# Kernel tuning notes

Hardware: AMD Instinct MI355X
Metric: run time of the kernel (lower is better)

## Reference

```python
import jax, jax.numpy as jnp
import numpy as np

B, T, E, L, V = 16, 1024, 768, 2, 50257
LN_EPS = 1e-5


def setup_inputs() -> dict:
    key = jax.random.key(0)
    ks = jax.random.split(key, 5)
    idx = jax.random.randint(ks[0], (B, T), 0, V)
    wte = jax.random.normal(ks[1], (V, E), dtype=jnp.float32) * 0.02
    Wih = jax.random.normal(ks[2], (L, 3 * E, E), dtype=jnp.float32) * 0.02
    Whh = jax.random.normal(ks[3], (L, 3 * E, E), dtype=jnp.float32) * 0.02
    bih = jnp.zeros((L, 3 * E), dtype=jnp.float32)
    bhh = jnp.zeros((L, 3 * E), dtype=jnp.float32)
    g = jnp.ones((E,), dtype=jnp.float32)
    return {"idx": idx, "wte": wte, "Wih": Wih, "bih": bih,
            "Whh": Whh, "bhh": bhh, "g": g}


def _gru_forward(idx, wte, Wih, bih, Whh, bhh, g):
    x = wte[idx]                       # [B,T,E] token embeddings (dropout=0 -> identity)

    def step(h, xt):                   # h: [L,B,E], xt: [B,E]
        inp = xt
        new_h = []
        for l in range(L):             # small fixed layer loop
            gi = inp @ Wih[l].T + bih[l]       # [B,3E]
            gh = h[l] @ Whh[l].T + bhh[l]      # [B,3E]
            i_r, i_z, i_n = jnp.split(gi, 3, axis=-1)
            h_r, h_z, h_n = jnp.split(gh, 3, axis=-1)
            r = jax.nn.sigmoid(i_r + h_r)
            z = jax.nn.sigmoid(i_z + h_z)
            n = jnp.tanh(i_n + r * h_n)
            hl = (1.0 - z) * n + z * h[l]
            new_h.append(hl)
            inp = hl
        return jnp.stack(new_h), inp   # carry, top-layer output at this t

    h0 = jnp.zeros((L, B, E), dtype=x.dtype)
    _, outs = jax.lax.scan(step, h0, jnp.swapaxes(x, 0, 1))  # outs: [T,B,E]

    # targets=None path: LayerNorm (no bias) + lm_head on the LAST position only
    last = outs[-1]                    # [B,E]
    mu = jnp.mean(last, axis=-1, keepdims=True)
    var = jnp.mean(jnp.square(last - mu), axis=-1, keepdims=True)
    ln = (last - mu) * jax.lax.rsqrt(var + LN_EPS) * g
    logits = ln @ wte.T                # tied lm_head, [B,V]
    return logits[:, None, :]          # [B,1,V]


def reference(idx, wte, Wih, bih, Whh, bhh, g):
    return _gru_forward(idx, wte, Wih, bih, Whh, bhh, g)
```

## Files before the change

kernel.cpp:

```cpp
#include <hip/hip_runtime.h>
#include <hip/hip_fp16.h>
#include <math.h>

#define Bz 16
#define Tz 1024
#define Ez 768
#define E3 2304
#define Vz 50257
#define NBK 256
#define LN_EPS 1e-5f
#define VEC (Bz*Ez)
#define VECW 6144
#define EP 772
#define BS 8
#define CW 12

__device__ __forceinline__ float dot4acc(float acc, float4 w, float4 h){
  acc = fmaf(w.x,h.x,acc); acc = fmaf(w.y,h.y,acc);
  acc = fmaf(w.z,h.z,acc); acc = fmaf(w.w,h.w,acc);
  return acc;
}
__device__ __forceinline__ float sigm(float x){ return 1.0f/(1.0f+expf(-x)); }

__device__ __forceinline__ unsigned pack2(float a, float b){
  __half2 h = __floats2half2_rn(a, b);
  union{__half2 h2; unsigned u;} cv; cv.h2 = h; return cv.u;
}
__device__ __forceinline__ float2 unpack2(unsigned u){
  union{unsigned u; __half2 h2;} cv; cv.u = u;
  return __half22float2(cv.h2);
}


__device__ __forceinline__ void stage8(const unsigned* __restrict__ src,
                                       float (*dst)[EP], int tid){
#pragma unroll
  for (int k=0;k<2;k++){
    const int u0 = tid + k*1536;
    const int u1 = u0 + 512;
    const int u2 = u0 + 1024;
    const unsigned a0 = __hip_atomic_load(src+u0, __ATOMIC_RELAXED, __HIP_MEMORY_SCOPE_AGENT);
    const unsigned a1 = __hip_atomic_load(src+u1, __ATOMIC_RELAXED, __HIP_MEMORY_SCOPE_AGENT);
    const unsigned a2 = __hip_atomic_load(src+u2, __ATOMIC_RELAXED, __HIP_MEMORY_SCOPE_AGENT);
    {const int b=u0/384, c=(u0-b*384)<<1; const float2 f=unpack2(a0); dst[b][c]=f.x; dst[b][c+1]=f.y;}
    {const int b=u1/384, c=(u1-b*384)<<1; const float2 f=unpack2(a1); dst[b][c]=f.x; dst[b][c+1]=f.y;}
    {const int b=u2/384, c=(u2-b*384)<<1; const float2 f=unpack2(a2); dst[b][c]=f.x; dst[b][c+1]=f.y;}
  }
}

__device__ __forceinline__ void zero8(float (*dst)[EP], int tid){
#pragma unroll
  for (int k=0;k<6;k++){
    const int u = tid + (k<<9);
    const int b = u/384, c = (u-b*384)<<1;
    dst[b][c] = 0.f; dst[b][c+1] = 0.f;
  }
}

__device__ __forceinline__ void mm6(const float (*V)[EP],
                                    const float* const (&wRow)[6],
                                    float (*gOut)[9],
                                    int wv, int kq, int bb){
  float acc[6][2];
#pragma unroll
  for (int r=0;r<6;r++){ acc[r][0]=0.f; acc[r][1]=0.f; }
#pragma unroll 4
  for (int j=0;j<12;j++){
    const int kk = (j<<6) + (kq<<2);
    float4 w4[6];
#pragma unroll
    for (int r=0;r<6;r++) w4[r] = *(const float4*)(wRow[r] + kk);
#pragma unroll
    for (int bi=0;bi<2;bi++){
      const float4 hv = *(const float4*)&V[bb*2+bi][kk];
#pragma unroll
      for (int r=0;r<6;r++) acc[r][bi] = dot4acc(acc[r][bi], w4[r], hv);
    }
  }
#pragma unroll
  for (int r=0;r<6;r++)
#pragma unroll
    for (int bi=0;bi<2;bi++){
      float a = acc[r][bi];
      a += __shfl_xor(a,1); a += __shfl_xor(a,2);
      a += __shfl_xor(a,4); a += __shfl_xor(a,8);
      acc[r][bi]=a;
    }
  if (kq==0){
#pragma unroll
    for (int r=0;r<6;r++)
#pragma unroll
      for (int bi=0;bi<2;bi++) gOut[wv*6+r][bb*2+bi] = acc[r][bi];
  }
}

__global__ __launch_bounds__(512) void gru_scan(
    const int* __restrict__ idx, const float* __restrict__ wte,
    const float* __restrict__ Wih, const float* __restrict__ bih,
    const float* __restrict__ Whh, const float* __restrict__ bhh,
    unsigned* __restrict__ h0g, unsigned* __restrict__ h1g,
    float* __restrict__ h1f,
    unsigned* __restrict__ flags, unsigned* __restrict__ go)
{
  __shared__ float bufX[BS][EP];
  __shared__ float bufH[BS][EP];
  __shared__ float gatesI[36][9];
  __shared__ float gatesG[36][9];
  __shared__ float biasS[72];
  __shared__ float hprev[BS][CW];

  const int tid = threadIdx.x, bx = blockIdx.x;
  const int L = bx>>7, sub = bx&127;
  const int bg = sub>>6, cg = sub&63;
  const int c0 = cg*CW, b0 = bg*BS;
  const int wv = tid>>6, lane = tid&63, kq = lane&15, bb = lane>>4;

  const float* WihL = Wih + (size_t)L*E3*Ez;
  const float* WhhL = Whh + (size_t)L*E3*Ez;

  const float* wiRow[6];
  const float* whRow[6];
#pragma unroll
  for (int r=0;r<6;r++){
    const int m = (wv<6 ? wv : 0)*6 + r, g = m/12, cc = m - g*12;
    wiRow[r] = WihL + (size_t)(g*Ez + c0 + cc)*Ez;
    whRow[r] = WhhL + (size_t)(g*Ez + c0 + cc)*Ez;
  }
  if (tid<72){
    const int mat = tid/36, mm = tid%36, g = mm/12, cc = mm-g*12;
    biasS[tid] = (mat ? bhh : bih)[L*E3 + g*Ez + c0 + cc];
  }
  if (tid<96) hprev[tid&7][tid>>3] = 0.f;

  if (L==0){
#pragma unroll
    for (int k=0;k<3;k++){
      const int i4 = tid + (k<<9);
      const int b = i4/192, c4 = i4 - b*192;
      const int row = idx[(b0+b)*Tz];
      *(float4*)&bufX[b][c4<<2] = *(const float4*)(wte + (size_t)row*Ez + (c4<<2));
    }
    __syncthreads();
    if (wv<6) mm6(bufX, wiRow, gatesI, wv, kq, bb);
  }
  __syncthreads();

  for (int s=0; s<=Tz+1; ++s){
    if (s>0){
      const unsigned tgt = (unsigned)s;
      if (bx==0){
        if (tid<64){
          const unsigned* f = flags + (tid<<2);
          for(;;){
            const unsigned a0 = __hip_atomic_load(f+0, __ATOMIC_RELAXED, __HIP_MEMORY_SCOPE_AGENT);
            const unsigned a1 = __hip_atomic_load(f+1, __ATOMIC_RELAXED, __HIP_MEMORY_SCOPE_AGENT);
            const unsigned a2 = __hip_atomic_load(f+2, __ATOMIC_RELAXED, __HIP_MEMORY_SCOPE_AGENT);
            const unsigned a3 = __hip_atomic_load(f+3, __ATOMIC_RELAXED, __HIP_MEMORY_SCOPE_AGENT);
            const int ok = (a0>=tgt) & (a1>=tgt) & (a2>=tgt) & (a3>=tgt);
            if (__all(ok)) break;
            __builtin_amdgcn_s_sleep(1);
          }
          __hip_atomic_store(go + (tid<<5), tgt,
                             __ATOMIC_RELAXED, __HIP_MEMORY_SCOPE_AGENT);
        }
      } else {
        if (tid==0){
          const unsigned* gp = go + ((bx&63)<<5);
          while (__hip_atomic_load(gp, __ATOMIC_RELAXED, __HIP_MEMORY_SCOPE_AGENT) < tgt)
            __builtin_amdgcn_s_sleep(2);
        }
      }
      __syncthreads();
    }

    const bool activeC = (L==0) ? (s<Tz) : (s>=2);
    if (activeC){
      if (L==0){
        if (s==0) zero8(bufH, tid);
        else      stage8(h0g + (size_t)((s-1)%3)*VECW + bg*3072, bufH, tid);
      } else {
        if (s==2) zero8(bufH, tid);
        else      stage8(h1g + (size_t)((s-1)&1)*VECW + bg*3072, bufH, tid);
      }
      __syncthreads();
      if (wv<6) mm6(bufH, whRow, gatesG, wv, kq, bb);
      __syncthreads();

      if (tid<48){
        const int b = tid&7, j = tid>>3;
        float hv2[2];
#pragma unroll
        for (int e=0;e<2;e++){
          const int cc = 2*j+e;
          const float gir = gatesI[cc    ][b] + biasS[cc];
          const float giz = gatesI[12+cc][b] + biasS[12+cc];
          const float gin = gatesI[24+cc][b] + biasS[24+cc];
          const float ghr = gatesG[cc    ][b] + biasS[36+cc];
          const float ghz = gatesG[12+cc][b] + biasS[48+cc];
          const float ghn = gatesG[24+cc][b] + biasS[60+cc];
          const float r = sigm(gir+ghr);
          const float z = sigm(giz+ghz);
          const float n = tanhf(fmaf(r, ghn, gin));
          const float hp = hprev[b][cc];
          hv2[e] = fmaf(z, hp - n, n);
          hprev[b][cc] = hv2[e];
        }
        unsigned* hOutW = (L==0) ? (h0g + (size_t)(s%3)*VECW)
                                 : (h1g + (size_t)(s&1)*VECW);
        const unsigned pk = pack2(hv2[0], hv2[1]);
        __hip_atomic_store(hOutW + (b0+b)*384 + cg*6 + j, pk,
                           __ATOMIC_RELAXED, __HIP_MEMORY_SCOPE_AGENT);
        if (L==1 && s==Tz+1){
          h1f[(b0+b)*Ez + c0 + 2*j    ] = hv2[0];
          h1f[(b0+b)*Ez + c0 + 2*j + 1] = hv2[1];
        }
      }
    }

    __syncthreads();
    if (tid==0)
      __hip_atomic_store(flags + bx, (unsigned)(s+1),
                         __ATOMIC_RELAXED, __HIP_MEMORY_SCOPE_AGENT);

    const bool activeE = (L==0) ? (s < Tz-1) : (s>=1 && s<=Tz);
    if (activeE){
      if (L==0){
#pragma unroll
        for (int k=0;k<3;k++){
          const int i4 = tid + (k<<9);
          const int b = i4/192, c4 = i4 - b*192;
          const int row = idx[(b0+b)*Tz + (s+1)];
          *(float4*)&bufX[b][c4<<2] = *(const float4*)(wte + (size_t)row*Ez + (c4<<2));
        }
      } else {
        stage8(h0g + (size_t)((s-1)%3)*VECW + bg*3072, bufX, tid);
      }
      __syncthreads();
      if (wv<6) mm6(bufX, wiRow, gatesI, wv, kq, bb);
    }
  }
}

__global__ __launch_bounds__(256) void finalize_ln(
    const float* __restrict__ h1, const float* __restrict__ g,
    float* __restrict__ ln)
{
  const int tid=threadIdx.x, wv=tid>>6, lane=tid&63;
  for (int b=wv; b<Bz; b+=4){
    float sum=0.f;
    for (int c=lane;c<Ez;c+=64) sum += h1[b*Ez+c];
#pragma unroll
    for (int off=32; off; off>>=1) sum += __shfl_xor(sum, off);
    const float mu = sum/(float)Ez;
    float s2=0.f;
    for (int c=lane;c<Ez;c+=64){ const float d=h1[b*Ez+c]-mu; s2=fmaf(d,d,s2); }
#pragma unroll
    for (int off=32; off; off>>=1) s2 += __shfl_xor(s2, off);
    const float inv = rsqrtf(s2/(float)Ez + LN_EPS);
    for (int c=lane;c<Ez;c+=64) ln[b*Ez+c] = (h1[b*Ez+c]-mu)*inv*g[c];
  }
}

__global__ __launch_bounds__(256) void lm_head(
    const float* __restrict__ ln, const float* __restrict__ wte,
    float* __restrict__ out)
{
  __shared__ float sLn[Bz][EP];
  const int tid=threadIdx.x;
  for (int i4=tid; i4<Bz*Ez/4; i4+=256){
    const int b = i4/(Ez/4), c = (i4 - b*(Ez/4))<<2;
    *(float4*)(&sLn[b][c]) = *(const float4*)(ln + b*Ez + c);
  }
  __syncthreads();
  const int wv=tid>>6, lane=tid&63, rr=lane>>4, cl=lane&15;
  const int vbase = blockIdx.x*64 + wv*16 + rr;
  float acc[4][16];
#pragma unroll
  for (int k=0;k<4;k++)
#pragma unroll
    for (int b=0;b<16;b++) acc[k][b]=0.f;

  for (int j=0;j<12;j++){
    const int c = (cl<<2) + (j<<6);
    float4 w4[4];
#pragma unroll
    for (int k=0;k<4;k++){
      const int v = vbase + 4*k;
      if (v < Vz) w4[k] = *(const float4*)(wte + (size_t)v*Ez + c);
      else { w4[k].x=w4[k].y=w4[k].z=w4[k].w=0.f; }
    }
#pragma unroll
    for (int b=0;b<16;b++){
      const float4 hv = *(const float4*)(&sLn[b][c]);
#pragma unroll
      for (int k=0;k<4;k++) acc[k][b] = dot4acc(acc[k][b], w4[k], hv);
    }
  }
#pragma unroll
  for (int off=1; off<16; off<<=1)
#pragma unroll
    for (int k=0;k<4;k++)
#pragma unroll
      for (int b=0;b<16;b++) acc[k][b] += __shfl_xor(acc[k][b], off);

  if (cl==0){
#pragma unroll
    for (int k=0;k<4;k++){
      const int v = vbase + 4*k;
      if (v < Vz){
#pragma unroll
        for (int b=0;b<16;b++) out[(size_t)b*Vz + v] = acc[k][b];
      }
    }
  }
}

extern "C" void kernel_launch(void* const* d_in, const int* in_sizes, int n_in,
                              void* d_out, int out_size, void* d_ws, size_t ws_size,
                              hipStream_t stream) {
  const int*   idx = (const int*)  d_in[0];
  const float* wte = (const float*)d_in[1];
  const float* Wih = (const float*)d_in[2];
  const float* bih = (const float*)d_in[3];
  const float* Whh = (const float*)d_in[4];
  const float* bhh = (const float*)d_in[5];
  const float* g   = (const float*)d_in[6];
  float* out = (float*)d_out;

  unsigned* flags = (unsigned*)d_ws;
  unsigned* go    = (unsigned*)d_ws + 512;
  unsigned* h0g   = (unsigned*)d_ws + 4096;
  unsigned* h1g   = h0g + 3*VECW;
  float*    h1f   = (float*)(h1g + 2*VECW);
  float*    ln    = h1f + VEC;

  (void)hipMemsetAsync(d_ws, 0, 16384, stream);

  void* args[] = {(void*)&idx,(void*)&wte,(void*)&Wih,(void*)&bih,
                  (void*)&Whh,(void*)&bhh,(void*)&h0g,(void*)&h1g,
                  (void*)&h1f,(void*)&flags,(void*)&go};
  (void)hipLaunchCooperativeKernel((void*)gru_scan, dim3(NBK), dim3(512), args, 0, stream);

  finalize_ln<<<1, 256, 0, stream>>>(h1f, g, ln);
  lm_head<<<786, 256, 0, stream>>>(ln, wte, out);
}
```

Baseline: 12.99 ms.

## Run input and hidden GEMVs concurrently on separate waves with double-buffered gates

All 8 waves now work each step: waves 0-3 compute the hidden-to-hidden gates (9 rows each) while waves 4-7 compute the input-to-hidden gates for the next step, using a double-buffered gatesI array. Before, only 6 waves ran, and they did the two matvecs one after the other. For layer 1 the staging of x and h is merged into one pass, and the layer-0 embedding prefetch moves one step further ahead. This shortens the serial critical path per step, at the cost of more complex step indexing and more registers for 9-row accumulators.

```diff
diff --git a/kernel.cpp b/kernel.cpp
--- a/kernel.cpp
+++ b/kernel.cpp
@@ -48,6 +48,27 @@
   }
 }
 
+__device__ __forceinline__ void stage8x2(const unsigned* __restrict__ srcX,
+                                         float (*dstX)[EP],
+                                         const unsigned* __restrict__ srcH,
+                                         float (*dstH)[EP], int tid){
+#pragma unroll
+  for (int k=0;k<3;k++){
+    const int u0 = tid + (k<<10);
+    const int u1 = u0 + 512;
+    const unsigned x0 = __hip_atomic_load(srcX+u0, __ATOMIC_RELAXED, __HIP_MEMORY_SCOPE_AGENT);
+    const unsigned x1 = __hip_atomic_load(srcX+u1, __ATOMIC_RELAXED, __HIP_MEMORY_SCOPE_AGENT);
+    const unsigned h0 = __hip_atomic_load(srcH+u0, __ATOMIC_RELAXED, __HIP_MEMORY_SCOPE_AGENT);
+    const unsigned h1 = __hip_atomic_load(srcH+u1, __ATOMIC_RELAXED, __HIP_MEMORY_SCOPE_AGENT);
+    const int b0=u0/384, c0_=(u0-b0*384)<<1;
+    const int b1=u1/384, c1_=(u1-b1*384)<<1;
+    {const float2 f=unpack2(x0); dstX[b0][c0_]=f.x; dstX[b0][c0_+1]=f.y;}
+    {const float2 f=unpack2(x1); dstX[b1][c1_]=f.x; dstX[b1][c1_+1]=f.y;}
+    {const float2 f=unpack2(h0); dstH[b0][c0_]=f.x; dstH[b0][c0_+1]=f.y;}
+    {const float2 f=unpack2(h1); dstH[b1][c1_]=f.x; dstH[b1][c1_+1]=f.y;}
+  }
+}
+
 __device__ __forceinline__ void zero8(float (*dst)[EP], int tid){
 #pragma unroll
   for (int k=0;k<6;k++){
@@ -57,28 +78,28 @@
   }
 }
 
-__device__ __forceinline__ void mm6(const float (*V)[EP],
-                                    const float* const (&wRow)[6],
+__device__ __forceinline__ void mm9(const float (*V)[EP],
+                                    const float* const (&wRow)[9],
                                     float (*gOut)[9],
-                                    int wv, int kq, int bb){
-  float acc[6][2];
-#pragma unroll
-  for (int r=0;r<6;r++){ acc[r][0]=0.f; acc[r][1]=0.f; }
+                                    int wv4, int kq, int bb){
+  float acc[9][2];
+#pragma unroll
+  for (int r=0;r<9;r++){ acc[r][0]=0.f; acc[r][1]=0.f; }
 #pragma unroll 4
   for (int j=0;j<12;j++){
     const int kk = (j<<6) + (kq<<2);
-    float4 w4[6];
-#pragma unroll
-    for (int r=0;r<6;r++) w4[r] = *(const float4*)(wRow[r] + kk);
+    float4 w4[9];
+#pragma unroll
+    for (int r=0;r<9;r++) w4[r] = *(const float4*)(wRow[r] + kk);
 #pragma unroll
     for (int bi=0;bi<2;bi++){
       const float4 hv = *(const float4*)&V[bb*2+bi][kk];
 #pragma unroll
-      for (int r=0;r<6;r++) acc[r][bi] = dot4acc(acc[r][bi], w4[r], hv);
-    }
-  }
-#pragma unroll
-  for (int r=0;r<6;r++)
+      for (int r=0;r<9;r++) acc[r][bi] = dot4acc(acc[r][bi], w4[r], hv);
+    }
+  }
+#pragma unroll
+  for (int r=0;r<9;r++)
 #pragma unroll
     for (int bi=0;bi<2;bi++){
       float a = acc[r][bi];
@@ -88,9 +109,9 @@
     }
   if (kq==0){
 #pragma unroll
-    for (int r=0;r<6;r++)
-#pragma unroll
-      for (int bi=0;bi<2;bi++) gOut[wv*6+r][bb*2+bi] = acc[r][bi];
+    for (int r=0;r<9;r++)
+#pragma unroll
+      for (int bi=0;bi<2;bi++) gOut[wv4*9+r][bb*2+bi] = acc[r][bi];
   }
 }
 
@@ -104,8 +125,8 @@
 {
   __shared__ float bufX[BS][EP];
   __shared__ float bufH[BS][EP];
-  __shared__ float gatesI[36][9];
   __shared__ float gatesG[36][9];
+  __shared__ float gatesI[2][36][9];
   __shared__ float biasS[72];
   __shared__ float hprev[BS][CW];
 
@@ -114,17 +135,19 @@
   const int bg = sub>>6, cg = sub&63;
   const int c0 = cg*CW, b0 = bg*BS;
   const int wv = tid>>6, lane = tid&63, kq = lane&15, bb = lane>>4;
+  const int wv4 = wv & 3;
 
   const float* WihL = Wih + (size_t)L*E3*Ez;
   const float* WhhL = Whh + (size_t)L*E3*Ez;
 
-  const float* wiRow[6];
-  const float* whRow[6];
-#pragma unroll
-  for (int r=0;r<6;r++){
-    const int m = (wv<6 ? wv : 0)*6 + r, g = m/12, cc = m - g*12;
-    wiRow[r] = WihL + (size_t)(g*Ez + c0 + cc)*Ez;
-    whRow[r] = WhhL + (size_t)(g*Ez + c0 + cc)*Ez;
+  const float* wRow[9];
+  {
+    const float* Wb = (wv < 4) ? WhhL : WihL;
+#pragma unroll
+    for (int r=0;r<9;r++){
+      const int m = wv4*9 + r, g = m/12, cc = m - g*12;
+      wRow[r] = Wb + (size_t)(g*Ez + c0 + cc)*Ez;
+    }
   }
   if (tid<72){
     const int mat = tid/36, mm = tid%36, g = mm/12, cc = mm-g*12;
@@ -141,7 +164,15 @@
       *(float4*)&bufX[b][c4<<2] = *(const float4*)(wte + (size_t)row*Ez + (c4<<2));
     }
     __syncthreads();
-    if (wv<6) mm6(bufX, wiRow, gatesI, wv, kq, bb);
+    if (wv>=4) mm9(bufX, wRow, gatesI[1], wv4, kq, bb);
+    __syncthreads();
+#pragma unroll
+    for (int k=0;k<3;k++){
+      const int i4 = tid + (k<<9);
+      const int b = i4/192, c4 = i4 - b*192;
+      const int row = idx[(b0+b)*Tz + 1];
+      *(float4*)&bufX[b][c4<<2] = *(const float4*)(wte + (size_t)row*Ez + (c4<<2));
+    }
   }
   __syncthreads();
 
@@ -173,44 +204,55 @@
       __syncthreads();
     }
 
-    const bool activeC = (L==0) ? (s<Tz) : (s>=2);
-    if (activeC){
+    const bool gG = (L==0) ? (s<=Tz-1) : (s>=2);
+    const bool gI = (L==0) ? (s<=Tz-2) : (s>=1 && s<=Tz);
+
+    if (L==0){
+      if (s==0)            zero8(bufH, tid);
+      else if (s<=Tz-1)    stage8(h0g + (size_t)((s-1)%3)*VECW + bg*3072, bufH, tid);
+    } else {
+      const unsigned* x_src = h0g + (size_t)((s-1)%3)*VECW + bg*3072;
+      const unsigned* h_src = h1g + (size_t)((s-1)&1)*VECW + bg*3072;
+      if (s>=3 && s<=Tz)      stage8x2(x_src, bufX, h_src, bufH, tid);
+      else if (s==2)        { stage8(x_src, bufX, tid); zero8(bufH, tid); }
+      else if (s==1)          stage8(x_src, bufX, tid);
+      else if (s==Tz+1)       stage8(h_src, bufH, tid);
+    }
+    __syncthreads();
+
+    if (wv<4){ if (gG) mm9(bufH, wRow, gatesG,        wv4, kq, bb); }
+    else     { if (gI) mm9(bufX, wRow, gatesI[s&1],   wv4, kq, bb); }
+    __syncthreads();
+
+    if (gG && tid<48){
+      const int b = tid&7, j = tid>>3;
+      float hv2[2];
+#pragma unroll
+      for (int e=0;e<2;e++){
+        const int cc = 2*j+e;
+        const float gir = gatesI[(s-1)&1][cc    ][b] + biasS[cc];
+        const float giz = gatesI[(s-1)&1][12+cc][b] + biasS[12+cc];
+        const float gin = gatesI[(s-1)&1][24+cc][b] + biasS[24+cc];
+        const float ghr = gatesG[cc    ][b] + biasS[36+cc];
+        const float ghz = gatesG[12+cc][b] + biasS[48+cc];
+        const float ghn = gatesG[24+cc][b] + biasS[60+cc];
+        const float r = sigm(gir+ghr);
+        const float z = sigm(giz+ghz);
+        const float n = tanhf(fmaf(r, ghn, gin));
+        const float hp = hprev[b][cc];
+        hv2[e] = fmaf(z, hp - n, n);
+        hprev[b][cc] = hv2[e];
+      }
+      const unsigned pk = pack2(hv2[0], hv2[1]);
       if (L==0){
-        if (s==0) zero8(bufH, tid);
-        else      stage8(h0g + (size_t)((s-1)%3)*VECW + bg*3072, bufH, tid);
-      } else {
-        if (s==2) zero8(bufH, tid);
-        else      stage8(h1g + (size_t)((s-1)&1)*VECW + bg*3072, bufH, tid);
-      }
-      __syncthreads();
-      if (wv<6) mm6(bufH, whRow, gatesG, wv, kq, bb);
-      __syncthreads();
-
-      if (tid<48){
-        const int b = tid&7, j = tid>>3;
-        float hv2[2];
-#pragma unroll
-        for (int e=0;e<2;e++){
-          const int cc = 2*j+e;
-          const float gir = gatesI[cc    ][b] + biasS[cc];
-          const float giz = gatesI[12+cc][b] + biasS[12+cc];
-          const float gin = gatesI[24+cc][b] + biasS[24+cc];
-          const float ghr = gatesG[cc    ][b] + biasS[36+cc];
-          const float ghz = gatesG[12+cc][b] + biasS[48+cc];
-          const float ghn = gatesG[24+cc][b] + biasS[60+cc];
-          const float r = sigm(gir+ghr);
-          const float z = sigm(giz+ghz);
-          const float n = tanhf(fmaf(r, ghn, gin));
-          const float hp = hprev[b][cc];
-          hv2[e] = fmaf(z, hp - n, n);
-          hprev[b][cc] = hv2[e];
-        }
-        unsigned* hOutW = (L==0) ? (h0g + (size_t)(s%3)*VECW)
-                                 : (h1g + (size_t)(s&1)*VECW);
-        const unsigned pk = pack2(hv2[0], hv2[1]);
+        unsigned* hOutW = h0g + (size_t)(s%3)*VECW;
         __hip_atomic_store(hOutW + (b0+b)*384 + cg*6 + j, pk,
                            __ATOMIC_RELAXED, __HIP_MEMORY_SCOPE_AGENT);
-        if (L==1 && s==Tz+1){
+      } else {
+        unsigned* hOutW = h1g + (size_t)((s-2)&1)*VECW;
+        __hip_atomic_store(hOutW + (b0+b)*384 + cg*6 + j, pk,
+                           __ATOMIC_RELAXED, __HIP_MEMORY_SCOPE_AGENT);
+        if (s==Tz+1){
           h1f[(b0+b)*Ez + c0 + 2*j    ] = hv2[0];
           h1f[(b0+b)*Ez + c0 + 2*j + 1] = hv2[1];
         }
@@ -222,21 +264,14 @@
       __hip_atomic_store(flags + bx, (unsigned)(s+1),
                          __ATOMIC_RELAXED, __HIP_MEMORY_SCOPE_AGENT);
 
-    const bool activeE = (L==0) ? (s < Tz-1) : (s>=1 && s<=Tz);
-    if (activeE){
-      if (L==0){
-#pragma unroll
-        for (int k=0;k<3;k++){
-          const int i4 = tid + (k<<9);
-          const int b = i4/192, c4 = i4 - b*192;
-          const int row = idx[(b0+b)*Tz + (s+1)];
-          *(float4*)&bufX[b][c4<<2] = *(const float4*)(wte + (size_t)row*Ez + (c4<<2));
-        }
-      } else {
-        stage8(h0g + (size_t)((s-1)%3)*VECW + bg*3072, bufX, tid);
-      }
-      __syncthreads();
-      if (wv<6) mm6(bufX, wiRow, gatesI, wv, kq, bb);
+    if (L==0 && s<=Tz-3){
+#pragma unroll
+      for (int k=0;k<3;k++){
+        const int i4 = tid + (k<<9);
+        const int b = i4/192, c4 = i4 - b*192;
+        const int row = idx[(b0+b)*Tz + (s+2)];
+        *(float4*)&bufX[b][c4<<2] = *(const float4*)(wte + (size_t)row*Ez + (c4<<2));
+      }
     }
   }
 }
```

Result: faster. 11.93 ms (-8.1%).
